# Optimization experiments

Hardware: AMD Instinct MI355X
Metric: run time of the kernel (lower is better)

The kernel has to match this reference:

```python
import jax, jax.numpy as jnp
import numpy as np

H = 16  # num_heads
B, N, M, D = 4, 512, 2048, 1024
FF = 4096  # mlp_ratio * D
LN_EPS = 1e-5


def _ln(x, g, b):
    m = x.mean(-1, keepdims=True)
    v = ((x - m) ** 2).mean(-1, keepdims=True)
    return (x - m) * jax.lax.rsqrt(v + LN_EPS) * g + b


def _attn(q_in, k_in, v_in, wq, bq, wk, bk, wv, bv, wp, bp):
    b, n, d = q_in.shape
    m = k_in.shape[1]
    hd = d // H
    scale = hd ** -0.5
    q = (q_in @ wq + bq).reshape(b, n, H, hd) * scale
    k = (k_in @ wk + bk).reshape(b, m, H, hd)
    v = (v_in @ wv + bv).reshape(b, m, H, hd)
    attn = jax.nn.softmax(jnp.einsum('bnhd,bmhd->bhnm', q, k), axis=-1)
    out = jnp.einsum('bhnm,bmhd->bnhd', attn, v).reshape(b, n, d)
    return out @ wp + bp


def setup_inputs() -> dict:
    key = jax.random.key(0)
    ks = iter(jax.random.split(key, 32))
    rnd = lambda shape: jax.random.normal(next(ks), shape, dtype=jnp.float32)
    w = lambda *shape: rnd(shape) * 0.02
    inp = {
        'state': rnd((B, N, D)),
        'patches': rnd((B, M, D)),
        'patches_pos_embed': rnd((B, M, D)),
        'state_query': rnd((B, N, D)),
    }
    for p in ('ca', 'sa'):
        inp[f'{p}_wq'] = w(D, D); inp[f'{p}_bq'] = jnp.zeros((D,), jnp.float32)
        inp[f'{p}_wk'] = w(D, D); inp[f'{p}_bk'] = jnp.zeros((D,), jnp.float32)
        inp[f'{p}_wv'] = w(D, D); inp[f'{p}_bv'] = jnp.zeros((D,), jnp.float32)
        inp[f'{p}_wp'] = w(D, D); inp[f'{p}_bp'] = jnp.zeros((D,), jnp.float32)
    inp['w1'] = w(D, FF); inp['b1'] = jnp.zeros((FF,), jnp.float32)
    inp['w2'] = w(FF, D); inp['b2'] = jnp.zeros((D,), jnp.float32)
    for i in (1, 2, 3):
        inp[f'n{i}_g'] = jnp.ones((D,), jnp.float32)
        inp[f'n{i}_b'] = jnp.zeros((D,), jnp.float32)
        inp[f'ls{i}'] = jnp.full((D,), 1e-5, jnp.float32)
    return inp


def reference(state, patches, patches_pos_embed, state_query,
              ca_wq, ca_bq, ca_wk, ca_bk, ca_wv, ca_bv, ca_wp, ca_bp,
              sa_wq, sa_bq, sa_wk, sa_bk, sa_wv, sa_bv, sa_wp, sa_bp,
              w1, b1, w2, b2,
              n1_g, n1_b, n2_g, n2_b, n3_g, n3_b,
              ls1, ls2, ls3):
    # pre-norm path of TransformerLayer.forward_pre (dropouts/drop_path = 0)
    state = state + state_query
    kv = patches + patches_pos_embed
    cross = _attn(_ln(state, n1_g, n1_b), kv, patches,
                  ca_wq, ca_bq, ca_wk, ca_bk, ca_wv, ca_bv, ca_wp, ca_bp)
    state = state + cross * ls1
    ns = _ln(state, n2_g, n2_b)
    selfa = _attn(ns, ns, ns,
                  sa_wq, sa_bq, sa_wk, sa_bk, sa_wv, sa_bv, sa_wp, sa_bp)
    state = state + selfa * ls2
    h = jax.nn.gelu(_ln(state, n3_g, n3_b) @ w1 + b1)
    return state + (h @ w2 + b2) * ls3
```

## Files before the change

### kernel.cpp

```cpp
#include <hip/hip_runtime.h>

#define DEV __device__ __forceinline__

typedef __bf16 bf16x8 __attribute__((ext_vector_type(8)));
typedef float f32x4 __attribute__((ext_vector_type(4)));

DEV unsigned short f2bf(float f) {
  __bf16 h = (__bf16)f;
  return __builtin_bit_cast(unsigned short, h);
}
DEV unsigned int cvtpk(float lo, float hi) {
  unsigned int r;
  asm("v_cvt_pk_bf16_f32 %0, %1, %2" : "=v"(r) : "v"(lo), "v"(hi));
  return r;
}

DEV void gload16(const void* g, void* l) {
  __builtin_amdgcn_global_load_lds(
      (const __attribute__((address_space(1))) unsigned int*)g,
      (__attribute__((address_space(3))) unsigned int*)l, 16, 0, 0);
}

DEV void tconv_body(const float* __restrict__ W, unsigned short* __restrict__ Wt,
                    int K, int N, int bx, int by) {
  __shared__ float tile[32][33];
  const int tx = threadIdx.x, ty = threadIdx.y;
  const int n0 = bx * 32, k0 = by * 32;
#pragma unroll
  for (int i = 0; i < 32; i += 8)
    tile[ty + i][tx] = W[(size_t)(k0 + ty + i) * N + n0 + tx];
  __syncthreads();
#pragma unroll
  for (int i = 0; i < 32; i += 8)
    Wt[(size_t)(n0 + ty + i) * K + k0 + tx] = f2bf(tile[tx][ty + i]);
}

__global__ __launch_bounds__(256) void tconv_kernel(
    const float* __restrict__ W, unsigned short* __restrict__ Wt, int K, int N) {
  tconv_body(W, Wt, K, N, blockIdx.x, blockIdx.y);
}

struct TC8 { const float* src[8]; unsigned short* dst[8]; };
__global__ __launch_bounds__(256) void tconv8_kernel(TC8 p) {
  tconv_body(p.src[blockIdx.z], p.dst[blockIdx.z], 1024, 1024, blockIdx.x, blockIdx.y);
}

__global__ __launch_bounds__(256) void cat3_kernel(
    const float* __restrict__ a, const float* __restrict__ b,
    const float* __restrict__ c, float* __restrict__ o) {
  const int i = blockIdx.x * 256 + threadIdx.x;
  o[i] = i < 1024 ? a[i] : (i < 2048 ? b[i - 1024] : c[i - 2048]);
}

__global__ __launch_bounds__(256) void vtrans_kernel(
    const unsigned short* __restrict__ V, unsigned short* __restrict__ vT,
    int Nk, int RS, int colbase) {
  __shared__ unsigned short tile[32][33];
  const int tx = threadIdx.x, ty = threadIdx.y;
  const int k0 = blockIdx.x * 32;
  const int h = blockIdx.y >> 1, dt = (blockIdx.y & 1) * 32;
  const int b = blockIdx.z;
#pragma unroll
  for (int i = 0; i < 32; i += 8)
    tile[ty + i][tx] = V[(size_t)(b * Nk + k0 + ty + i) * RS + colbase + h * 64 + dt + tx];
  __syncthreads();
#pragma unroll
  for (int i = 0; i < 32; i += 8)
    vT[((size_t)(b * 16 + h) * 64 + dt + ty + i) * Nk + k0 + tx] = tile[tx][ty + i];
}

__global__ __launch_bounds__(256) void add_ln_kernel(
    const float* __restrict__ a, const float* b, float* x0_out,
    unsigned short* __restrict__ y, const float* __restrict__ gam,
    const float* __restrict__ bet) {
  const int row = blockIdx.x, t = threadIdx.x;
  const int c = t * 4;
  const size_t base = (size_t)row * 1024 + c;
  float4 v = *reinterpret_cast<const float4*>(a + base);
  if (b) {
    float4 v2 = *reinterpret_cast<const float4*>(b + base);
    v.x += v2.x; v.y += v2.y; v.z += v2.z; v.w += v2.w;
  }
  if (x0_out) *reinterpret_cast<float4*>(x0_out + base) = v;
  float s = v.x + v.y + v.z + v.w;
  float sq = v.x * v.x + v.y * v.y + v.z * v.z + v.w * v.w;
#pragma unroll
  for (int o = 32; o > 0; o >>= 1) {
    s += __shfl_xor(s, o);
    sq += __shfl_xor(sq, o);
  }
  __shared__ float ps[4], pq[4];
  const int w = t >> 6;
  if ((t & 63) == 0) { ps[w] = s; pq[w] = sq; }
  __syncthreads();
  s = ps[0] + ps[1] + ps[2] + ps[3];
  sq = pq[0] + pq[1] + pq[2] + pq[3];
  const float mean = s * (1.f / 1024.f);
  const float var = sq * (1.f / 1024.f) - mean * mean;
  const float rstd = rsqrtf(var + 1e-5f);
  float4 gv = *reinterpret_cast<const float4*>(gam + c);
  float4 bv = *reinterpret_cast<const float4*>(bet + c);
  uint2 o2;
  o2.x = cvtpk((v.x - mean) * rstd * gv.x + bv.x, (v.y - mean) * rstd * gv.y + bv.y);
  o2.y = cvtpk((v.z - mean) * rstd * gv.z + bv.z, (v.w - mean) * rstd * gv.w + bv.w);
  *reinterpret_cast<uint2*>(y + base) = o2;
}

__global__ __launch_bounds__(256) void kvcast_kernel(
    const float* __restrict__ p, const float* __restrict__ pe,
    unsigned short* __restrict__ kvo, unsigned short* __restrict__ po) {
  const size_t i = ((size_t)blockIdx.x * 256 + threadIdx.x) * 4;
  float4 a = *reinterpret_cast<const float4*>(p + i);
  float4 b = *reinterpret_cast<const float4*>(pe + i);
  uint2 kv2, p2;
  kv2.x = cvtpk(a.x + b.x, a.y + b.y);
  kv2.y = cvtpk(a.z + b.z, a.w + b.w);
  p2.x = cvtpk(a.x, a.y);
  p2.y = cvtpk(a.z, a.w);
  *reinterpret_cast<uint2*>(kvo + i) = kv2;
  *reinterpret_cast<uint2*>(po + i) = p2;
}

template <int EPI, int BM, int BN>
__global__ __launch_bounds__(256) void gemm_kernel(
    const unsigned short* __restrict__ A, const unsigned short* __restrict__ Bt,
    const float* __restrict__ bias, const float* resid,
    const float* __restrict__ ls, void* outp, int M, int N, int K, int lda) {
  constexpr int WM = BM / 32;
  constexpr int WN = BN / 32;
  __shared__ __align__(16) unsigned short As[2][BM * 32];
  __shared__ __align__(16) unsigned short Bs[2][BN * 32];
  const int t = threadIdx.x;
  const int lane = t & 63, w = t >> 6;
  const int wr = w >> 1, wc = w & 1;
  const int g = lane >> 4, lr = lane & 15;
  const int srow = lane >> 2, scol = (lane & 3) * 8;

  const int gx = gridDim.x, gy = gridDim.y;
  const int gxy = gx * gy;
  const int nwg = gxy * gridDim.z;
  const int orig = (blockIdx.z * gy + blockIdx.y) * gx + blockIdx.x;
  const int q = nwg >> 3, r = nwg & 7;
  const int xcd = orig & 7;
  int wgid = (xcd < r ? xcd * (q + 1) : r * (q + 1) + (xcd - r) * q) + (orig >> 3);
  const int bz = wgid / gxy;
  wgid -= bz * gxy;
  int bx, by;
  if (gy >= gx) { by = wgid / gx; bx = wgid - by * gx; }
  else          { bx = wgid / gy; by = wgid - bx * gy; }
  const int brow = by * BM, bcol = bx * BN;
  const int koff = bz * K;

  f32x4 acc[WM][WN] = {};

  auto stage = [&](int buf, int k0) {
#pragma unroll
    for (int i = 0; i < BM / 64; i++) {
      const int r0 = (i * 4 + w) * 16;
      gload16(A + (size_t)(brow + r0 + srow) * lda + koff + k0 + scol, &As[buf][r0 * 32]);
    }
#pragma unroll
    for (int i = 0; i < BN / 64; i++) {
      const int r0 = (i * 4 + w) * 16;
      gload16(Bt + (size_t)(bcol + r0 + srow) * lda + koff + k0 + scol, &Bs[buf][r0 * 32]);
    }
  };

  stage(0, 0);
  const int nk = K / 32;
  int cur = 0;
  for (int kt = 0; kt < nk; kt++) {
    __syncthreads();
    if (kt + 1 < nk) stage(cur ^ 1, (kt + 1) * 32);
    bf16x8 af[WM], bfr[WN];
#pragma unroll
    for (int m = 0; m < WM; m++)
      af[m] = *reinterpret_cast<const bf16x8*>(
          &As[cur][(wr * (BM / 2) + m * 16 + lr) * 32 + g * 8]);
#pragma unroll
    for (int n = 0; n < WN; n++)
      bfr[n] = *reinterpret_cast<const bf16x8*>(
          &Bs[cur][(wc * (BN / 2) + n * 16 + lr) * 32 + g * 8]);
#pragma unroll
    for (int m = 0; m < WM; m++)
#pragma unroll
      for (int n = 0; n < WN; n++)
        acc[m][n] = __builtin_amdgcn_mfma_f32_16x16x32_bf16(af[m], bfr[n], acc[m][n], 0, 0, 0);
    cur ^= 1;
  }

#pragma unroll
  for (int m = 0; m < WM; m++) {
    const int row0 = brow + wr * (BM / 2) + m * 16 + g * 4;
#pragma unroll
    for (int n = 0; n < WN; n++) {
      const int col = bcol + wc * (BN / 2) + n * 16 + lr;
      const float bv = (EPI == 4) ? 0.f : bias[col];
#pragma unroll
      for (int r = 0; r < 4; r++) {
        const float v = acc[m][n][r] + bv;
        const size_t idx = (size_t)(row0 + r) * N + col;
        if (EPI == 0) {
          ((unsigned short*)outp)[idx] = f2bf(v);
        } else if (EPI == 2) {
          ((float*)outp)[idx] = resid[idx] + v * ls[col];
        } else if (EPI == 3) {
          const float tth = tanhf(0.7978845608028654f * (v + 0.044715f * v * v * v));
          ((unsigned short*)outp)[idx] = f2bf(0.5f * v * (1.f + tth));
        } else {
          ((float*)outp)[(size_t)bz * M * N + idx] = v;
        }
      }
    }
  }
}

__global__ __launch_bounds__(256) void splitk_red_kernel(
    const float* __restrict__ p, const float* __restrict__ bias,
    const float* __restrict__ resid, const float* __restrict__ ls,
    float* __restrict__ out) {
  const size_t i = ((size_t)blockIdx.x * 256 + threadIdx.x) * 4;
  const int c = (int)(i & 1023);
  float4 a = *reinterpret_cast<const float4*>(p + i);
  float4 b = *reinterpret_cast<const float4*>(p + 2048ull * 1024 + i);
  float4 rv = *reinterpret_cast<const float4*>(resid + i);
  float4 bb = *reinterpret_cast<const float4*>(bias + c);
  float4 lv = *reinterpret_cast<const float4*>(ls + c);
  float4 o;
  o.x = rv.x + (a.x + b.x + bb.x) * lv.x;
  o.y = rv.y + (a.y + b.y + bb.y) * lv.y;
  o.z = rv.z + (a.z + b.z + bb.z) * lv.z;
  o.w = rv.w + (a.w + b.w + bb.w) * lv.w;
  *reinterpret_cast<float4*>(out + i) = o;
}

__global__ __launch_bounds__(256) void attn_kernel(
    const unsigned short* __restrict__ Q, const unsigned short* __restrict__ Kp,
    const unsigned short* __restrict__ vT, unsigned short* __restrict__ O,
    int RSq, int RSk, int Nq, int Nk, float k2 ) {
  __shared__ __align__(16) unsigned short Qs[64 * 72];
  __shared__ __align__(16) unsigned short Ks[2][64 * 72];
  __shared__ __align__(16) unsigned short Vs[2][64 * 72];
  __shared__ __align__(16) unsigned short Ps[64 * 72];
  const int t = threadIdx.x, lane = t & 63, w = t >> 6;
  const int qt = blockIdx.y, h = blockIdx.x & 15, b = blockIdx.x >> 4;
  const int g = lane >> 4, lr = lane & 15;
  const int srow = t >> 2, scol = (t & 3) * 16;

  {
    const uint4* gq = reinterpret_cast<const uint4*>(
        Q + (size_t)(b * Nq + qt * 64 + srow) * RSq + h * 64 + scol);
    *reinterpret_cast<uint4*>(&Qs[srow * 72 + scol]) = gq[0];
    *reinterpret_cast<uint4*>(&Qs[srow * 72 + scol + 8]) = gq[1];
  }
  float m_i = -1e30f, l_i = 0.f;
  f32x4 acc_o[4] = {};

  auto kaddr = [&](int kv0) {
    return reinterpret_cast<const uint4*>(
        Kp + (size_t)(b * Nk + kv0 + srow) * RSk + h * 64 + scol);
  };
  auto vaddr = [&](int kv0) {
    return reinterpret_cast<const uint4*>(
        vT + ((size_t)(b * 16 + h) * 64 + srow) * Nk + kv0 + scol);
  };

  uint4 kr0 = kaddr(0)[0], kr1 = kaddr(0)[1];
  uint4 vr0 = vaddr(0)[0], vr1 = vaddr(0)[1];

  int cur = 0;
  for (int kv0 = 0; kv0 < Nk; kv0 += 64) {
    *reinterpret_cast<uint4*>(&Ks[cur][srow * 72 + scol]) = kr0;
    *reinterpret_cast<uint4*>(&Ks[cur][srow * 72 + scol + 8]) = kr1;
    *reinterpret_cast<uint4*>(&Vs[cur][srow * 72 + scol]) = vr0;
    *reinterpret_cast<uint4*>(&Vs[cur][srow * 72 + scol + 8]) = vr1;
    __syncthreads();
    if (kv0 + 64 < Nk) {
      kr0 = kaddr(kv0 + 64)[0]; kr1 = kaddr(kv0 + 64)[1];
      vr0 = vaddr(kv0 + 64)[0]; vr1 = vaddr(kv0 + 64)[1];
    }

    f32x4 accs[4] = {};
    __builtin_amdgcn_s_setprio(1);
#pragma unroll
    for (int d0 = 0; d0 < 64; d0 += 32) {
      bf16x8 qf = *reinterpret_cast<const bf16x8*>(&Qs[(w * 16 + lr) * 72 + d0 + g * 8]);
#pragma unroll
      for (int m = 0; m < 4; m++) {
        bf16x8 kf = *reinterpret_cast<const bf16x8*>(&Ks[cur][(m * 16 + lr) * 72 + d0 + g * 8]);
        accs[m] = __builtin_amdgcn_mfma_f32_16x16x32_bf16(kf, qf, accs[m], 0, 0, 0);
      }
    }
    __builtin_amdgcn_s_setprio(0);
    float pmax = -1e30f;
#pragma unroll
    for (int m = 0; m < 4; m++)
#pragma unroll
      for (int r = 0; r < 4; r++) pmax = fmaxf(pmax, accs[m][r]);
    pmax = fmaxf(pmax, __shfl_xor(pmax, 16));
    pmax = fmaxf(pmax, __shfl_xor(pmax, 32));
    const float pm2 = pmax * k2;
    if (!__all(pm2 <= m_i + 8.f)) {
      const float m_new = fmaxf(m_i, pm2);
      const float corr = exp2f(m_i - m_new);
      m_i = m_new;
      l_i *= corr;
#pragma unroll
      for (int r = 0; r < 4; r++) {
        const float cf = __shfl(corr, g * 4 + r);
#pragma unroll
        for (int n = 0; n < 4; n++) acc_o[n][r] *= cf;
      }
    }
    float psum = 0.f;
#pragma unroll
    for (int m = 0; m < 4; m++) {
      float p0 = exp2f(fmaf(accs[m][0], k2, -m_i));
      float p1 = exp2f(fmaf(accs[m][1], k2, -m_i));
      float p2 = exp2f(fmaf(accs[m][2], k2, -m_i));
      float p3 = exp2f(fmaf(accs[m][3], k2, -m_i));
      psum += p0 + p1 + p2 + p3;
      uint2 pk;
      pk.x = cvtpk(p0, p1);
      pk.y = cvtpk(p2, p3);
      *reinterpret_cast<uint2*>(&Ps[(w * 16 + lr) * 72 + m * 16 + g * 4]) = pk;
    }
    psum += __shfl_xor(psum, 16);
    psum += __shfl_xor(psum, 32);
    l_i += psum;
    __builtin_amdgcn_s_setprio(1);
#pragma unroll
    for (int ks = 0; ks < 2; ks++) {
      bf16x8 pf = *reinterpret_cast<const bf16x8*>(&Ps[(w * 16 + lr) * 72 + ks * 32 + g * 8]);
#pragma unroll
      for (int n = 0; n < 4; n++) {
        bf16x8 vf = *reinterpret_cast<const bf16x8*>(&Vs[cur][(n * 16 + lr) * 72 + ks * 32 + g * 8]);
        acc_o[n] = __builtin_amdgcn_mfma_f32_16x16x32_bf16(pf, vf, acc_o[n], 0, 0, 0);
      }
    }
    __builtin_amdgcn_s_setprio(0);
    cur ^= 1;
  }
#pragma unroll
  for (int r = 0; r < 4; r++) {
    const float li = __shfl(l_i, g * 4 + r);
    const float inv = 1.f / li;
    const int qrow = qt * 64 + w * 16 + g * 4 + r;
#pragma unroll
    for (int n = 0; n < 4; n++)
      O[(size_t)(b * Nq + qrow) * 1024 + h * 64 + n * 16 + lr] = f2bf(acc_o[n][r] * inv);
  }
}

extern "C" void kernel_launch(void* const* d_in, const int* in_sizes, int n_in,
                              void* d_out, int out_size, void* d_ws, size_t ws_size,
                              hipStream_t stream) {
  const float* state = (const float*)d_in[0];
  const float* patches = (const float*)d_in[1];
  const float* ppe = (const float*)d_in[2];
  const float* squery = (const float*)d_in[3];
  const float* ca_wq = (const float*)d_in[4];
  const float* ca_bq = (const float*)d_in[5];
  const float* ca_wk = (const float*)d_in[6];
  const float* ca_bk = (const float*)d_in[7];
  const float* ca_wv = (const float*)d_in[8];
  const float* ca_bv = (const float*)d_in[9];
  const float* ca_wp = (const float*)d_in[10];
  const float* ca_bp = (const float*)d_in[11];
  const float* sa_wq = (const float*)d_in[12];
  const float* sa_bq = (const float*)d_in[13];
  const float* sa_wk = (const float*)d_in[14];
  const float* sa_bk = (const float*)d_in[15];
  const float* sa_wv = (const float*)d_in[16];
  const float* sa_bv = (const float*)d_in[17];
  const float* sa_wp = (const float*)d_in[18];
  const float* sa_bp = (const float*)d_in[19];
  const float* w1 = (const float*)d_in[20];
  const float* b1 = (const float*)d_in[21];
  const float* w2 = (const float*)d_in[22];
  const float* b2 = (const float*)d_in[23];
  const float* n1_g = (const float*)d_in[24];
  const float* n1_b = (const float*)d_in[25];
  const float* ls1 = (const float*)d_in[26];
  const float* n2_g = (const float*)d_in[27];
  const float* n2_b = (const float*)d_in[28];
  const float* ls2 = (const float*)d_in[29];
  const float* n3_g = (const float*)d_in[30];
  const float* n3_b = (const float*)d_in[31];
  const float* ls3 = (const float*)d_in[32];

  char* wsp = (char*)d_ws;
  auto alloc = [&](size_t bytes) {
    void* p = (void*)wsp;
    wsp += (bytes + 255) & ~(size_t)255;
    return p;
  };
  float* stateF = (float*)alloc(2048ull * 1024 * 4);
  unsigned short* lnB = (unsigned short*)alloc(2048ull * 1024 * 2);
  unsigned short* kvB = (unsigned short*)alloc(8192ull * 1024 * 2);
  unsigned short* patB = (unsigned short*)alloc(8192ull * 1024 * 2);
  unsigned short* qB = (unsigned short*)alloc(2048ull * 1024 * 2);
  unsigned short* kB = (unsigned short*)alloc(8192ull * 1024 * 2);
  unsigned short* vB = (unsigned short*)alloc(8192ull * 1024 * 2);
  unsigned short* oB = (unsigned short*)alloc(2048ull * 1024 * 2);
  unsigned short* hB = kvB;
  unsigned short* qkvB = kB;
  unsigned short* vTc = patB;
  unsigned short* vTs = qB;
  float* mlp2p = (float*)patB;
  unsigned short* ca_wqt = (unsigned short*)alloc(1024ull * 1024 * 2);
  unsigned short* ca_wkt = (unsigned short*)alloc(1024ull * 1024 * 2);
  unsigned short* ca_wvt = (unsigned short*)alloc(1024ull * 1024 * 2);
  unsigned short* ca_wpt = (unsigned short*)alloc(1024ull * 1024 * 2);
  unsigned short* sa_wqkvt = (unsigned short*)alloc(3072ull * 1024 * 2);
  unsigned short* sa_wpt = (unsigned short*)alloc(1024ull * 1024 * 2);
  unsigned short* w1t = (unsigned short*)alloc(4096ull * 1024 * 2);
  unsigned short* w2t = (unsigned short*)alloc(4096ull * 1024 * 2);
  float* sa_bqkv = (float*)alloc(3072 * 4);

  const dim3 tb(32, 8);
  TC8 tc;
  tc.src[0] = ca_wq; tc.dst[0] = ca_wqt;
  tc.src[1] = ca_wk; tc.dst[1] = ca_wkt;
  tc.src[2] = ca_wv; tc.dst[2] = ca_wvt;
  tc.src[3] = ca_wp; tc.dst[3] = ca_wpt;
  tc.src[4] = sa_wq; tc.dst[4] = sa_wqkvt;
  tc.src[5] = sa_wk; tc.dst[5] = sa_wqkvt + 1024ull * 1024;
  tc.src[6] = sa_wv; tc.dst[6] = sa_wqkvt + 2048ull * 1024;
  tc.src[7] = sa_wp; tc.dst[7] = sa_wpt;
  tconv8_kernel<<<dim3(32, 32, 8), tb, 0, stream>>>(tc);
  tconv_kernel<<<dim3(128, 32), tb, 0, stream>>>(w1, w1t, 1024, 4096);
  tconv_kernel<<<dim3(32, 128), tb, 0, stream>>>(w2, w2t, 4096, 1024);
  cat3_kernel<<<12, 256, 0, stream>>>(sa_bq, sa_bk, sa_bv, sa_bqkv);

  add_ln_kernel<<<2048, 256, 0, stream>>>(state, squery, stateF, lnB, n1_g, n1_b);
  kvcast_kernel<<<8192, 256, 0, stream>>>(patches, ppe, kvB, patB);

  const float k2 = 0.125f * 1.4426950408889634f;
  gemm_kernel<0, 64, 64><<<dim3(16, 32), 256, 0, stream>>>(lnB, ca_wqt, ca_bq, nullptr, nullptr, qB, 2048, 1024, 1024, 1024);
  gemm_kernel<0, 128, 64><<<dim3(16, 64), 256, 0, stream>>>(kvB, ca_wkt, ca_bk, nullptr, nullptr, kB, 8192, 1024, 1024, 1024);
  gemm_kernel<0, 128, 64><<<dim3(16, 64), 256, 0, stream>>>(patB, ca_wvt, ca_bv, nullptr, nullptr, vB, 8192, 1024, 1024, 1024);
  vtrans_kernel<<<dim3(64, 32, 4), tb, 0, stream>>>(vB, vTc, 2048, 1024, 0);
  attn_kernel<<<dim3(64, 8), 256, 0, stream>>>(qB, kB, vTc, oB, 1024, 1024, 512, 2048, k2);
  gemm_kernel<2, 64, 64><<<dim3(16, 32), 256, 0, stream>>>(oB, ca_wpt, ca_bp, stateF, ls1, stateF, 2048, 1024, 1024, 1024);

  add_ln_kernel<<<2048, 256, 0, stream>>>(stateF, nullptr, nullptr, lnB, n2_g, n2_b);
  gemm_kernel<0, 128, 64><<<dim3(48, 16), 256, 0, stream>>>(lnB, sa_wqkvt, sa_bqkv, nullptr, nullptr, qkvB, 2048, 3072, 1024, 1024);
  vtrans_kernel<<<dim3(16, 32, 4), tb, 0, stream>>>(qkvB, vTs, 512, 3072, 2048);
  attn_kernel<<<dim3(64, 8), 256, 0, stream>>>(qkvB, qkvB + 1024, vTs, oB, 3072, 3072, 512, 512, k2);
  gemm_kernel<2, 64, 64><<<dim3(16, 32), 256, 0, stream>>>(oB, sa_wpt, sa_bp, stateF, ls2, stateF, 2048, 1024, 1024, 1024);

  add_ln_kernel<<<2048, 256, 0, stream>>>(stateF, nullptr, nullptr, lnB, n3_g, n3_b);
  gemm_kernel<3, 128, 64><<<dim3(64, 16), 256, 0, stream>>>(lnB, w1t, b1, nullptr, nullptr, hB, 2048, 4096, 1024, 1024);
  gemm_kernel<4, 64, 64><<<dim3(16, 32, 2), 256, 0, stream>>>(hB, w2t, nullptr, nullptr, nullptr, mlp2p, 2048, 1024, 2048, 4096);
  splitk_red_kernel<<<2048, 256, 0, stream>>>(mlp2p, b2, stateF, ls3, (float*)d_out);
}
```

Before: 336.8 us.

## Group cross-attention projections, widen attention tiles, enlarge MLP GEMM tiles

Merges the three cross-attention Q/K/V projection GEMMs into one grouped launch using 128x128 tiles and a shared XCD swizzle helper. Attention now runs 512-thread blocks covering 128 query rows, keeping Q in registers and dropping the Q shared buffer. The MLP GEMM tile sizes grow (128x128 for w1, 128x64 for split-K w2). These are meant to cut launch count and raise per-tile reuse, at the cost of more registers and shared memory per block and fewer blocks in flight.

```diff
diff --git a/kernel.cpp b/kernel.cpp
--- a/kernel.cpp
+++ b/kernel.cpp
@@ -121,6 +121,19 @@
   *reinterpret_cast<uint2*>(po + i) = p2;
 }
 
+DEV void xcd_swizzle(int gx, int gy, int& bx, int& by, int& bz) {
+  const int gxy = gx * gy;
+  const int nwg = gxy * gridDim.z;
+  const int orig = (blockIdx.z * gy + blockIdx.y) * gx + blockIdx.x;
+  const int q = nwg >> 3, r = nwg & 7;
+  const int xcd = orig & 7;
+  int wgid = (xcd < r ? xcd * (q + 1) : r * (q + 1) + (xcd - r) * q) + (orig >> 3);
+  bz = wgid / gxy;
+  wgid -= bz * gxy;
+  if (gy >= gx) { by = wgid / gx; bx = wgid - by * gx; }
+  else          { bx = wgid / gy; by = wgid - bx * gy; }
+}
+
 template <int EPI, int BM, int BN>
 __global__ __launch_bounds__(256) void gemm_kernel(
     const unsigned short* __restrict__ A, const unsigned short* __restrict__ Bt,
@@ -136,18 +149,8 @@
   const int g = lane >> 4, lr = lane & 15;
   const int srow = lane >> 2, scol = (lane & 3) * 8;
 
-  const int gx = gridDim.x, gy = gridDim.y;
-  const int gxy = gx * gy;
-  const int nwg = gxy * gridDim.z;
-  const int orig = (blockIdx.z * gy + blockIdx.y) * gx + blockIdx.x;
-  const int q = nwg >> 3, r = nwg & 7;
-  const int xcd = orig & 7;
-  int wgid = (xcd < r ? xcd * (q + 1) : r * (q + 1) + (xcd - r) * q) + (orig >> 3);
-  const int bz = wgid / gxy;
-  wgid -= bz * gxy;
-  int bx, by;
-  if (gy >= gx) { by = wgid / gx; bx = wgid - by * gx; }
-  else          { bx = wgid / gy; by = wgid - bx * gy; }
+  int bx, by, bz;
+  xcd_swizzle(gridDim.x, gridDim.y, bx, by, bz);
   const int brow = by * BM, bcol = bx * BN;
   const int koff = bz * K;
 
@@ -211,6 +214,76 @@
           ((float*)outp)[(size_t)bz * M * N + idx] = v;
         }
       }
+    }
+  }
+}
+
+struct G3 {
+  const unsigned short* A[3]; const unsigned short* Bt[3];
+  const float* bias[3]; unsigned short* out[3]; int ecum[3];
+};
+__global__ __launch_bounds__(256) void gemm3_kernel(G3 p, int N, int K) {
+  constexpr int BM = 128, BN = 128, WM = 4, WN = 4;
+  __shared__ __align__(16) unsigned short As[2][BM * 32];
+  __shared__ __align__(16) unsigned short Bs[2][BN * 32];
+  const int t = threadIdx.x;
+  const int lane = t & 63, w = t >> 6;
+  const int wr = w >> 1, wc = w & 1;
+  const int g = lane >> 4, lr = lane & 15;
+  const int srow = lane >> 2, scol = (lane & 3) * 8;
+
+  int bx, by, bz;
+  xcd_swizzle(gridDim.x, gridDim.y, bx, by, bz);
+  const int s = (by >= p.ecum[0]) + (by >= p.ecum[1]);
+  const int byloc = by - (s ? p.ecum[s - 1] : 0);
+  const unsigned short* A = p.A[s];
+  const unsigned short* Bt = p.Bt[s];
+  const float* bias = p.bias[s];
+  unsigned short* outp = p.out[s];
+  const int brow = byloc * BM, bcol = bx * BN;
+
+  f32x4 acc[WM][WN] = {};
+
+  auto stage = [&](int buf, int k0) {
+#pragma unroll
+    for (int i = 0; i < 2; i++) {
+      const int r0 = (i * 4 + w) * 16;
+      gload16(A + (size_t)(brow + r0 + srow) * K + k0 + scol, &As[buf][r0 * 32]);
+      gload16(Bt + (size_t)(bcol + r0 + srow) * K + k0 + scol, &Bs[buf][r0 * 32]);
+    }
+  };
+
+  stage(0, 0);
+  const int nk = K / 32;
+  int cur = 0;
+  for (int kt = 0; kt < nk; kt++) {
+    __syncthreads();
+    if (kt + 1 < nk) stage(cur ^ 1, (kt + 1) * 32);
+    bf16x8 af[WM], bfr[WN];
+#pragma unroll
+    for (int m = 0; m < WM; m++)
+      af[m] = *reinterpret_cast<const bf16x8*>(&As[cur][(wr * 64 + m * 16 + lr) * 32 + g * 8]);
+#pragma unroll
+    for (int n = 0; n < WN; n++)
+      bfr[n] = *reinterpret_cast<const bf16x8*>(&Bs[cur][(wc * 64 + n * 16 + lr) * 32 + g * 8]);
+#pragma unroll
+    for (int m = 0; m < WM; m++)
+#pragma unroll
+      for (int n = 0; n < WN; n++)
+        acc[m][n] = __builtin_amdgcn_mfma_f32_16x16x32_bf16(af[m], bfr[n], acc[m][n], 0, 0, 0);
+    cur ^= 1;
+  }
+
+#pragma unroll
+  for (int m = 0; m < WM; m++) {
+    const int row0 = brow + wr * 64 + m * 16 + g * 4;
+#pragma unroll
+    for (int n = 0; n < WN; n++) {
+      const int col = bcol + wc * 64 + n * 16 + lr;
+      const float bv = bias[col];
+#pragma unroll
+      for (int r = 0; r < 4; r++)
+        outp[(size_t)(row0 + r) * N + col] = f2bf(acc[m][n][r] + bv);
     }
   }
 }
@@ -234,24 +307,23 @@
   *reinterpret_cast<float4*>(out + i) = o;
 }
 
-__global__ __launch_bounds__(256) void attn_kernel(
+__global__ __launch_bounds__(512) void attn_kernel(
     const unsigned short* __restrict__ Q, const unsigned short* __restrict__ Kp,
     const unsigned short* __restrict__ vT, unsigned short* __restrict__ O,
-    int RSq, int RSk, int Nq, int Nk, float k2 ) {
-  __shared__ __align__(16) unsigned short Qs[64 * 72];
+    int RSq, int RSk, int Nq, int Nk, float k2) {
   __shared__ __align__(16) unsigned short Ks[2][64 * 72];
   __shared__ __align__(16) unsigned short Vs[2][64 * 72];
-  __shared__ __align__(16) unsigned short Ps[64 * 72];
+  __shared__ __align__(16) unsigned short Ps[128 * 72];
   const int t = threadIdx.x, lane = t & 63, w = t >> 6;
   const int qt = blockIdx.y, h = blockIdx.x & 15, b = blockIdx.x >> 4;
   const int g = lane >> 4, lr = lane & 15;
-  const int srow = t >> 2, scol = (t & 3) * 16;
-
+  const int srow = t >> 3, scol = (t & 7) * 8;
+
+  uint4 qr[2];
   {
-    const uint4* gq = reinterpret_cast<const uint4*>(
-        Q + (size_t)(b * Nq + qt * 64 + srow) * RSq + h * 64 + scol);
-    *reinterpret_cast<uint4*>(&Qs[srow * 72 + scol]) = gq[0];
-    *reinterpret_cast<uint4*>(&Qs[srow * 72 + scol + 8]) = gq[1];
+    const unsigned short* qp = Q + (size_t)(b * Nq + qt * 128 + w * 16 + lr) * RSq + h * 64 + g * 8;
+    qr[0] = *reinterpret_cast<const uint4*>(qp);
+    qr[1] = *reinterpret_cast<const uint4*>(qp + 32);
   }
   float m_i = -1e30f, l_i = 0.f;
   f32x4 acc_o[4] = {};
@@ -265,26 +337,24 @@
         vT + ((size_t)(b * 16 + h) * 64 + srow) * Nk + kv0 + scol);
   };
 
-  uint4 kr0 = kaddr(0)[0], kr1 = kaddr(0)[1];
-  uint4 vr0 = vaddr(0)[0], vr1 = vaddr(0)[1];
+  uint4 kr = kaddr(0)[0];
+  uint4 vr = vaddr(0)[0];
 
   int cur = 0;
   for (int kv0 = 0; kv0 < Nk; kv0 += 64) {
-    *reinterpret_cast<uint4*>(&Ks[cur][srow * 72 + scol]) = kr0;
-    *reinterpret_cast<uint4*>(&Ks[cur][srow * 72 + scol + 8]) = kr1;
-    *reinterpret_cast<uint4*>(&Vs[cur][srow * 72 + scol]) = vr0;
-    *reinterpret_cast<uint4*>(&Vs[cur][srow * 72 + scol + 8]) = vr1;
+    *reinterpret_cast<uint4*>(&Ks[cur][srow * 72 + scol]) = kr;
+    *reinterpret_cast<uint4*>(&Vs[cur][srow * 72 + scol]) = vr;
     __syncthreads();
     if (kv0 + 64 < Nk) {
-      kr0 = kaddr(kv0 + 64)[0]; kr1 = kaddr(kv0 + 64)[1];
-      vr0 = vaddr(kv0 + 64)[0]; vr1 = vaddr(kv0 + 64)[1];
+      kr = kaddr(kv0 + 64)[0];
+      vr = vaddr(kv0 + 64)[0];
     }
 
     f32x4 accs[4] = {};
     __builtin_amdgcn_s_setprio(1);
 #pragma unroll
     for (int d0 = 0; d0 < 64; d0 += 32) {
-      bf16x8 qf = *reinterpret_cast<const bf16x8*>(&Qs[(w * 16 + lr) * 72 + d0 + g * 8]);
+      bf16x8 qf = __builtin_bit_cast(bf16x8, qr[d0 >> 5]);
 #pragma unroll
       for (int m = 0; m < 4; m++) {
         bf16x8 kf = *reinterpret_cast<const bf16x8*>(&Ks[cur][(m * 16 + lr) * 72 + d0 + g * 8]);
@@ -345,7 +415,7 @@
   for (int r = 0; r < 4; r++) {
     const float li = __shfl(l_i, g * 4 + r);
     const float inv = 1.f / li;
-    const int qrow = qt * 64 + w * 16 + g * 4 + r;
+    const int qrow = qt * 128 + w * 16 + g * 4 + r;
 #pragma unroll
     for (int n = 0; n < 4; n++)
       O[(size_t)(b * Nq + qrow) * 1024 + h * 64 + n * 16 + lr] = f2bf(acc_o[n][r] * inv);
@@ -437,21 +507,24 @@
   kvcast_kernel<<<8192, 256, 0, stream>>>(patches, ppe, kvB, patB);
 
   const float k2 = 0.125f * 1.4426950408889634f;
-  gemm_kernel<0, 64, 64><<<dim3(16, 32), 256, 0, stream>>>(lnB, ca_wqt, ca_bq, nullptr, nullptr, qB, 2048, 1024, 1024, 1024);
-  gemm_kernel<0, 128, 64><<<dim3(16, 64), 256, 0, stream>>>(kvB, ca_wkt, ca_bk, nullptr, nullptr, kB, 8192, 1024, 1024, 1024);
-  gemm_kernel<0, 128, 64><<<dim3(16, 64), 256, 0, stream>>>(patB, ca_wvt, ca_bv, nullptr, nullptr, vB, 8192, 1024, 1024, 1024);
+
+  G3 g3;
+  g3.A[0] = lnB;  g3.Bt[0] = ca_wqt; g3.bias[0] = ca_bq; g3.out[0] = qB;  g3.ecum[0] = 16;
+  g3.A[1] = kvB;  g3.Bt[1] = ca_wkt; g3.bias[1] = ca_bk; g3.out[1] = kB;  g3.ecum[1] = 80;
+  g3.A[2] = patB; g3.Bt[2] = ca_wvt; g3.bias[2] = ca_bv; g3.out[2] = vB;  g3.ecum[2] = 144;
+  gemm3_kernel<<<dim3(8, 144), 256, 0, stream>>>(g3, 1024, 1024);
   vtrans_kernel<<<dim3(64, 32, 4), tb, 0, stream>>>(vB, vTc, 2048, 1024, 0);
-  attn_kernel<<<dim3(64, 8), 256, 0, stream>>>(qB, kB, vTc, oB, 1024, 1024, 512, 2048, k2);
+  attn_kernel<<<dim3(64, 4), 512, 0, stream>>>(qB, kB, vTc, oB, 1024, 1024, 512, 2048, k2);
   gemm_kernel<2, 64, 64><<<dim3(16, 32), 256, 0, stream>>>(oB, ca_wpt, ca_bp, stateF, ls1, stateF, 2048, 1024, 1024, 1024);
 
   add_ln_kernel<<<2048, 256, 0, stream>>>(stateF, nullptr, nullptr, lnB, n2_g, n2_b);
   gemm_kernel<0, 128, 64><<<dim3(48, 16), 256, 0, stream>>>(lnB, sa_wqkvt, sa_bqkv, nullptr, nullptr, qkvB, 2048, 3072, 1024, 1024);
   vtrans_kernel<<<dim3(16, 32, 4), tb, 0, stream>>>(qkvB, vTs, 512, 3072, 2048);
-  attn_kernel<<<dim3(64, 8), 256, 0, stream>>>(qkvB, qkvB + 1024, vTs, oB, 3072, 3072, 512, 512, k2);
+  attn_kernel<<<dim3(64, 4), 512, 0, stream>>>(qkvB, qkvB + 1024, vTs, oB, 3072, 3072, 512, 512, k2);
   gemm_kernel<2, 64, 64><<<dim3(16, 32), 256, 0, stream>>>(oB, sa_wpt, sa_bp, stateF, ls2, stateF, 2048, 1024, 1024, 1024);
 
   add_ln_kernel<<<2048, 256, 0, stream>>>(stateF, nullptr, nullptr, lnB, n3_g, n3_b);
-  gemm_kernel<3, 128, 64><<<dim3(64, 16), 256, 0, stream>>>(lnB, w1t, b1, nullptr, nullptr, hB, 2048, 4096, 1024, 1024);
-  gemm_kernel<4, 64, 64><<<dim3(16, 32, 2), 256, 0, stream>>>(hB, w2t, nullptr, nullptr, nullptr, mlp2p, 2048, 1024, 2048, 4096);
+  gemm_kernel<3, 128, 128><<<dim3(32, 16), 256, 0, stream>>>(lnB, w1t, b1, nullptr, nullptr, hB, 2048, 4096, 1024, 1024);
+  gemm_kernel<4, 128, 64><<<dim3(16, 16, 2), 256, 0, stream>>>(hB, w2t, nullptr, nullptr, nullptr, mlp2p, 2048, 1024, 2048, 4096);
   splitk_red_kernel<<<2048, 256, 0, stream>>>(mlp2p, b2, stateF, ls3, (float*)d_out);
 }
```

Measured after the change: 318.1 us. 5.6% less time.
